# Optimization experiments

Measured on AMD Instinct MI355X. Metric: run time of the kernel, lower is better.

The kernel has to match this reference:

```python
import jax, jax.numpy as jnp
import numpy as np

B, I, H, S = 16384, 256, 256, 32
EVENT_THRESH = 0.85


def setup_inputs() -> dict:
    key = jax.random.key(0)
    ks = jax.random.split(key, 20)
    r = lambda k, shp: jax.random.normal(k, shp, dtype=jnp.float32)
    w = lambda k, shp: jax.random.normal(k, shp, dtype=jnp.float32) * 0.02
    return {
        # forward args / state
        "x_t": r(ks[0], (B, I)),
        "h_lstm": r(ks[1], (B, H)),
        "c_lstm": r(ks[2], (B, H)),
        "h_mem_prev": jnp.zeros((B, H), jnp.float32),
        "slots": r(ks[3], (B, S, I)),
        "ptr": jax.random.randint(ks[4], (B,), 0, S, dtype=jnp.int64),
        # SequenceMemoryCell params (weights stored as (in, out))
        "W_val": w(ks[5], (I, I)),
        "b_val": jnp.zeros((I,), jnp.float32),
        "W_ev": w(ks[6], (I, 1)),
        "b_ev": jnp.zeros((1,), jnp.float32),
        "pos_emb": r(ks[7], (S, I)),
        "slot_weights": jnp.ones((S,), jnp.float32),
        "W_sp": w(ks[8], (I, H)),
        "b_sp": jnp.zeros((H,), jnp.float32),
        # LSTM params
        "W_ih": w(ks[9], (I + H, 4 * H)),
        "b_ih": jnp.zeros((4 * H,), jnp.float32),
        "W_hh": w(ks[10], (H, 4 * H)),
    }


def reference(x_t, h_lstm, c_lstm, h_mem_prev, slots, ptr,
              W_val, b_val, W_ev, b_ev, pos_emb, slot_weights, W_sp, b_sp,
              W_ih, b_ih, W_hh):
    n_slots = slot_weights.shape[0]
    # --- SequenceMemoryCell ---
    e_t = jax.nn.sigmoid(x_t @ W_ev + b_ev)            # (B, 1)
    v = x_t @ W_val + b_val                            # (B, I)
    event_mask = e_t[:, 0] > EVENT_THRESH              # (B,)
    # circular-buffer scatter write at ptr, gated by event_mask
    onehot = jnp.arange(n_slots)[None, :] == ptr[:, None]          # (B, S)
    write = event_mask[:, None] & onehot                           # (B, S)
    new_slots = jnp.where(write[:, :, None], v[:, None, :], slots) # (B, S, I)
    new_ptr = (ptr + event_mask.astype(ptr.dtype)) % n_slots
    # weighted pool over slots with positional embeddings
    w = jax.nn.softmax(slot_weights)                               # (S,)
    pooled = jnp.einsum('bsi,s->bi', new_slots + pos_emb[None], w) # (B, I)
    h_mem = pooled @ W_sp + b_sp                                   # (B, H)
    # --- LSTM on [x_t; h_mem] ---
    gates = jnp.concatenate([x_t, h_mem], axis=1) @ W_ih + b_ih + h_lstm @ W_hh
    i_g, f_g, g_t, o_g = jnp.split(gates, 4, axis=1)
    c_new = jax.nn.sigmoid(f_g) * c_lstm + jax.nn.sigmoid(i_g) * jnp.tanh(g_t)
    h_new = jax.nn.sigmoid(o_g) * jnp.tanh(c_new)
    return (h_new, c_new, h_mem, new_slots, new_ptr)
```

## Files before the change

### kernel.cpp

```cpp
#include <hip/hip_runtime.h>
#include <hip/hip_bf16.h>

#define B_SZ 16384
#define I_SZ 256
#define H_SZ 256
#define S_SZ 32

typedef __attribute__((ext_vector_type(8))) short short8;
typedef __attribute__((ext_vector_type(4))) float f32x4;
typedef __attribute__((ext_vector_type(4))) short s16x4;

__device__ __forceinline__ ushort f2b(float f) {
  __hip_bfloat16 h = __float2bfloat16(f);
  return *reinterpret_cast<ushort*>(&h);
}
__device__ __forceinline__ float b2f(ushort u) {
  unsigned x = ((unsigned)u) << 16;
  float f;
  __builtin_memcpy(&f, &x, 4);
  return f;
}
__device__ __forceinline__ float sgm(float x) { return 1.0f / (1.0f + expf(-x)); }

__device__ __forceinline__ void gll16(const void* g, void* l) {
  __builtin_amdgcn_global_load_lds(
      (const __attribute__((address_space(1))) unsigned*)g,
      (__attribute__((address_space(3))) unsigned*)l, 16, 0, 0);
}

__global__ __launch_bounds__(256) void prep_weights(
    const float* __restrict__ W_sp, const float* __restrict__ W_ih,
    const float* __restrict__ W_hh, ushort* __restrict__ WspT,
    ushort* __restrict__ WcatT) {
  int idx = blockIdx.x * 256 + threadIdx.x;
  if (idx < 256 * 256) {
    int n = idx >> 8, k = idx & 255;
    WspT[idx] = f2b(W_sp[k * 256 + n]);
  } else {
    int j = idx - 256 * 256;
    int n = j / 768, k = j - n * 768;
    float v = (k < 512) ? W_ih[k * 1024 + n] : W_hh[(k - 512) * 1024 + n];
    WcatT[j] = f2b(v);
  }
}

__global__ __launch_bounds__(256) void event_pool(
    const float* __restrict__ x_t, const float* __restrict__ h_lstm,
    const float* __restrict__ slots, const int* __restrict__ ptr,
    const float* __restrict__ W_val, const float* __restrict__ b_val,
    const float* __restrict__ W_ev, const float* __restrict__ b_ev,
    const float* __restrict__ pos_emb, const float* __restrict__ slot_w,
    float* __restrict__ out_slots, float* __restrict__ out_ptr,
    ushort* __restrict__ x_b, ushort* __restrict__ hl_b,
    ushort* __restrict__ pooled_b) {
  int l = threadIdx.x & 63;
  int w = threadIdx.x >> 6;
  int b = blockIdx.x * 4 + w;
  __shared__ float x_sh[4][256];

  float4 x4 = *(const float4*)(x_t + (size_t)b * 256 + l * 4);
  *(float4*)&x_sh[w][l * 4] = x4;
  ushort4 xb = make_ushort4(f2b(x4.x), f2b(x4.y), f2b(x4.z), f2b(x4.w));
  *(ushort4*)&x_b[(size_t)b * 256 + l * 4] = xb;
  float4 hl4 = *(const float4*)(h_lstm + (size_t)b * 256 + l * 4);
  ushort4 hb = make_ushort4(f2b(hl4.x), f2b(hl4.y), f2b(hl4.z), f2b(hl4.w));
  *(ushort4*)&hl_b[(size_t)b * 256 + l * 4] = hb;

  float4 we4 = *(const float4*)(W_ev + l * 4);
  float p = x4.x * we4.x + x4.y * we4.y + x4.z * we4.z + x4.w * we4.w;
  for (int off = 32; off; off >>= 1) p += __shfl_xor(p, off, 64);
  float z = p + b_ev[0];
  bool ev = sgm(z) > 0.85f;
  int pb = ptr[b];

  __syncthreads();

  float4 v4 = make_float4(0.f, 0.f, 0.f, 0.f);
  if (ev) {
    v4 = *(const float4*)(b_val + l * 4);
    for (int k = 0; k < 256; k++) {
      float xv = x_sh[w][k];
      float4 wv = *(const float4*)(W_val + (size_t)k * 256 + l * 4);
      v4.x += xv * wv.x; v4.y += xv * wv.y;
      v4.z += xv * wv.z; v4.w += xv * wv.w;
    }
  }

  float mx = -1e30f;
  for (int s = 0; s < 32; s++) mx = fmaxf(mx, slot_w[s]);
  float sum = 0.f;
  for (int s = 0; s < 32; s++) sum += expf(slot_w[s] - mx);
  float rs = 1.f / sum;

  const float4* sl4 = (const float4*)slots + (size_t)b * 2048;
  float4* os4 = (float4*)out_slots + (size_t)b * 2048;
  const float4* pe4 = (const float4*)pos_emb;
  float4 pool = make_float4(0.f, 0.f, 0.f, 0.f);
#pragma unroll 8
  for (int s = 0; s < 32; s++) {
    float ws_ = expf(slot_w[s] - mx) * rs;
    float4 t = sl4[s * 64 + l];
    if (ev && s == pb) t = v4;
    os4[s * 64 + l] = t;
    float4 pe = pe4[s * 64 + l];
    pool.x += ws_ * (t.x + pe.x);
    pool.y += ws_ * (t.y + pe.y);
    pool.z += ws_ * (t.z + pe.z);
    pool.w += ws_ * (t.w + pe.w);
  }
  ushort4 pb4 = make_ushort4(f2b(pool.x), f2b(pool.y), f2b(pool.z), f2b(pool.w));
  *(ushort4*)&pooled_b[(size_t)b * 256 + l * 4] = pb4;

  if (l == 0) out_ptr[b] = (float)(ev ? ((pb + 1) & 31) : pb);
}

template <int KTOT, int NTOT, int EPI>
__global__ __launch_bounds__(256) void gemm_bf16(
    const ushort* __restrict__ A0, const ushort* __restrict__ A1,
    const ushort* __restrict__ A2, const ushort* __restrict__ WT,
    const float* __restrict__ bias, float* __restrict__ out_f32,
    ushort* __restrict__ out_b16) {
  int l = threadIdx.x & 63;
  int wid = threadIdx.x >> 6;
  int wm = wid >> 1, wn = wid & 1;
  int m0 = blockIdx.x * 128;
  int n0 = blockIdx.y * 128;
  __shared__ ushort Ash[128 * 32];
  __shared__ ushort Bsh[128 * 32];

  f32x4 acc[4][4] = {};

  for (int k0 = 0; k0 < KTOT; k0 += 32) {
    const ushort* As = (k0 < 256) ? A0 : ((k0 < 512) ? A1 : A2);
    int kc = k0 & 255;
#pragma unroll
    for (int i = 0; i < 2; i++) {
      int seg = i * 256 + threadIdx.x;
      int row = seg >> 2, cb = (seg & 3) * 8;
      gll16(As + (size_t)(m0 + row) * 256 + kc + cb, Ash + seg * 8);
    }
#pragma unroll
    for (int i = 0; i < 2; i++) {
      int seg = i * 256 + threadIdx.x;
      int row = seg >> 2, cb = (seg & 3) * 8;
      gll16(WT + (size_t)(n0 + row) * KTOT + k0 + cb, Bsh + seg * 8);
    }
    __syncthreads();

    short8 af[4], bfr[4];
#pragma unroll
    for (int m = 0; m < 4; m++)
      af[m] = *(const short8*)&Ash[(wm * 64 + m * 16 + (l & 15)) * 32 + (l >> 4) * 8];
#pragma unroll
    for (int n = 0; n < 4; n++)
      bfr[n] = *(const short8*)&Bsh[(wn * 64 + n * 16 + (l & 15)) * 32 + (l >> 4) * 8];
#pragma unroll
    for (int m = 0; m < 4; m++)
#pragma unroll
      for (int n = 0; n < 4; n++)
        acc[m][n] = __builtin_amdgcn_mfma_f32_16x16x32_bf16(af[m], bfr[n], acc[m][n], 0, 0, 0);
    __syncthreads();
  }

#pragma unroll
  for (int m = 0; m < 4; m++)
#pragma unroll
    for (int n = 0; n < 4; n++)
#pragma unroll
      for (int r = 0; r < 4; r++) {
        int row = m0 + wm * 64 + m * 16 + (l >> 4) * 4 + r;
        int col = n0 + wn * 64 + n * 16 + (l & 15);
        float v = acc[m][n][r] + bias[col];
        if constexpr (EPI == 0) {
          out_f32[(size_t)row * NTOT + col] = v;
          out_b16[(size_t)row * NTOT + col] = f2b(v);
        } else {
          out_b16[(size_t)row * NTOT + col] = f2b(v);
        }
      }
}

__global__ __launch_bounds__(256) void lstm_ew(
    const ushort* __restrict__ gates, const float* __restrict__ c_lstm,
    float* __restrict__ h_out, float* __restrict__ c_out) {
  int t = blockIdx.x * 256 + threadIdx.x;
  int b = t >> 6;
  int h4 = (t & 63) * 4;
  size_t g0 = (size_t)b * 1024 + h4;
  s16x4 ig = *(const s16x4*)&gates[g0];
  s16x4 fg = *(const s16x4*)&gates[g0 + 256];
  s16x4 gg = *(const s16x4*)&gates[g0 + 512];
  s16x4 og = *(const s16x4*)&gates[g0 + 768];
  float4 c = *(const float4*)&c_lstm[(size_t)b * 256 + h4];
  float4 cn, hn;
  {
    float i0 = sgm(b2f((ushort)ig[0])), f0 = sgm(b2f((ushort)fg[0]));
    float g0v = tanhf(b2f((ushort)gg[0])), o0 = sgm(b2f((ushort)og[0]));
    cn.x = f0 * c.x + i0 * g0v; hn.x = o0 * tanhf(cn.x);
  }
  {
    float i1 = sgm(b2f((ushort)ig[1])), f1 = sgm(b2f((ushort)fg[1]));
    float g1 = tanhf(b2f((ushort)gg[1])), o1 = sgm(b2f((ushort)og[1]));
    cn.y = f1 * c.y + i1 * g1; hn.y = o1 * tanhf(cn.y);
  }
  {
    float i2 = sgm(b2f((ushort)ig[2])), f2 = sgm(b2f((ushort)fg[2]));
    float g2 = tanhf(b2f((ushort)gg[2])), o2 = sgm(b2f((ushort)og[2]));
    cn.z = f2 * c.z + i2 * g2; hn.z = o2 * tanhf(cn.z);
  }
  {
    float i3 = sgm(b2f((ushort)ig[3])), f3 = sgm(b2f((ushort)fg[3]));
    float g3 = tanhf(b2f((ushort)gg[3])), o3 = sgm(b2f((ushort)og[3]));
    cn.w = f3 * c.w + i3 * g3; hn.w = o3 * tanhf(cn.w);
  }
  size_t o = (size_t)b * 256 + h4;
  *(float4*)&c_out[o] = cn;
  *(float4*)&h_out[o] = hn;
}

extern "C" void kernel_launch(void* const* d_in, const int* in_sizes, int n_in,
                              void* d_out, int out_size, void* d_ws, size_t ws_size,
                              hipStream_t stream) {
  const float* x_t    = (const float*)d_in[0];
  const float* h_lstm = (const float*)d_in[1];
  const float* c_lstm = (const float*)d_in[2];
  const float* slots  = (const float*)d_in[4];
  const int*   ptr    = (const int*)d_in[5];
  const float* W_val  = (const float*)d_in[6];
  const float* b_val  = (const float*)d_in[7];
  const float* W_ev   = (const float*)d_in[8];
  const float* b_ev   = (const float*)d_in[9];
  const float* pos_emb = (const float*)d_in[10];
  const float* slot_w  = (const float*)d_in[11];
  const float* W_sp   = (const float*)d_in[12];
  const float* b_sp   = (const float*)d_in[13];
  const float* W_ih   = (const float*)d_in[14];
  const float* b_ih   = (const float*)d_in[15];
  const float* W_hh   = (const float*)d_in[16];

  float* out = (float*)d_out;
  const size_t BH = (size_t)B_SZ * H_SZ;
  float* out_h    = out;
  float* out_c    = out + BH;
  float* out_hmem = out + 2 * BH;
  float* out_slots = out + 3 * BH;
  float* out_ptr   = out + 3 * BH + (size_t)B_SZ * S_SZ * I_SZ;

  char* ws = (char*)d_ws;
  ushort* x_b      = (ushort*)(ws);
  ushort* hl_b     = (ushort*)(ws + 8388608);
  ushort* pooled_b = (ushort*)(ws + 16777216);
  ushort* hmem_b   = (ushort*)(ws + 25165824);
  ushort* WspT     = (ushort*)(ws + 33554432);
  ushort* WcatT    = (ushort*)(ws + 33685504);
  ushort* gates    = (ushort*)(ws + 35258368);

  prep_weights<<<3328, 256, 0, stream>>>(W_sp, W_ih, W_hh, WspT, WcatT);

  event_pool<<<B_SZ / 4, 256, 0, stream>>>(
      x_t, h_lstm, slots, ptr, W_val, b_val, W_ev, b_ev, pos_emb, slot_w,
      out_slots, out_ptr, x_b, hl_b, pooled_b);

  gemm_bf16<256, 256, 0><<<dim3(128, 2), 256, 0, stream>>>(
      pooled_b, pooled_b, pooled_b, WspT, b_sp, out_hmem, hmem_b);

  gemm_bf16<768, 1024, 1><<<dim3(128, 8), 256, 0, stream>>>(
      x_b, hmem_b, hl_b, WcatT, b_ih, nullptr, gates);

  lstm_ew<<<B_SZ * 64 / 256, 256, 0, stream>>>(gates, c_lstm, out_h, out_c);
}
```

Before: 309.0 us.

## Fuse LSTM elementwise into gate GEMM epilogue via interleaved weight columns

Reorders the columns of the concatenated LSTM weight so each wave's 64-column slice holds the i, f, g and o gates for the same 16 hidden units. The LSTM cell update can then run directly in the GEMM epilogue, which removes the bf16 gates buffer round-trip and the separate lstm_ew launch. Gates now stay in fp32 rather than being rounded to bf16. The epilogue now reads c_lstm and writes h and c with 16-lane strided scalar accesses, which are less coalesced than the old float4 accesses.

Result: no change. 304.9 us (-1.3%).

```diff
diff --git a/kernel.cpp b/kernel.cpp
--- a/kernel.cpp
+++ b/kernel.cpp
@@ -8,17 +8,10 @@
 
 typedef __attribute__((ext_vector_type(8))) short short8;
 typedef __attribute__((ext_vector_type(4))) float f32x4;
-typedef __attribute__((ext_vector_type(4))) short s16x4;
 
 __device__ __forceinline__ ushort f2b(float f) {
   __hip_bfloat16 h = __float2bfloat16(f);
   return *reinterpret_cast<ushort*>(&h);
-}
-__device__ __forceinline__ float b2f(ushort u) {
-  unsigned x = ((unsigned)u) << 16;
-  float f;
-  __builtin_memcpy(&f, &x, 4);
-  return f;
 }
 __device__ __forceinline__ float sgm(float x) { return 1.0f / (1.0f + expf(-x)); }
 
@@ -38,7 +31,9 @@
     WspT[idx] = f2b(W_sp[k * 256 + n]);
   } else {
     int j = idx - 256 * 256;
-    int n = j / 768, k = j - n * 768;
+    int r = j / 768, k = j - r * 768;
+    int hb = r >> 6, g = (r >> 4) & 3, hl = r & 15;
+    int n = g * 256 + hb * 16 + hl;
     float v = (k < 512) ? W_ih[k * 1024 + n] : W_hh[(k - 512) * 1024 + n];
     WcatT[j] = f2b(v);
   }
@@ -119,7 +114,8 @@
     const ushort* __restrict__ A0, const ushort* __restrict__ A1,
     const ushort* __restrict__ A2, const ushort* __restrict__ WT,
     const float* __restrict__ bias, float* __restrict__ out_f32,
-    ushort* __restrict__ out_b16) {
+    ushort* __restrict__ out_b16, const float* __restrict__ c_lstm,
+    float* __restrict__ h_out, float* __restrict__ c_out) {
   int l = threadIdx.x & 63;
   int wid = threadIdx.x >> 6;
   int wm = wid >> 1, wn = wid & 1;
@@ -162,60 +158,38 @@
     __syncthreads();
   }
 
-#pragma unroll
-  for (int m = 0; m < 4; m++)
-#pragma unroll
-    for (int n = 0; n < 4; n++)
+  if constexpr (EPI == 0) {
+#pragma unroll
+    for (int m = 0; m < 4; m++)
+#pragma unroll
+      for (int n = 0; n < 4; n++)
+#pragma unroll
+        for (int r = 0; r < 4; r++) {
+          int row = m0 + wm * 64 + m * 16 + (l >> 4) * 4 + r;
+          int col = n0 + wn * 64 + n * 16 + (l & 15);
+          float v = acc[m][n][r] + bias[col];
+          out_f32[(size_t)row * NTOT + col] = v;
+          out_b16[(size_t)row * NTOT + col] = f2b(v);
+        }
+  } else {
+    int h = ((n0 >> 6) + wn) * 16 + (l & 15);
+    float bi = bias[h], bf_ = bias[256 + h], bg = bias[512 + h], bo = bias[768 + h];
+#pragma unroll
+    for (int m = 0; m < 4; m++)
 #pragma unroll
       for (int r = 0; r < 4; r++) {
         int row = m0 + wm * 64 + m * 16 + (l >> 4) * 4 + r;
-        int col = n0 + wn * 64 + n * 16 + (l & 15);
-        float v = acc[m][n][r] + bias[col];
-        if constexpr (EPI == 0) {
-          out_f32[(size_t)row * NTOT + col] = v;
-          out_b16[(size_t)row * NTOT + col] = f2b(v);
-        } else {
-          out_b16[(size_t)row * NTOT + col] = f2b(v);
-        }
+        float ig = acc[m][0][r] + bi;
+        float fg = acc[m][1][r] + bf_;
+        float gt = acc[m][2][r] + bg;
+        float og = acc[m][3][r] + bo;
+        float c = c_lstm[(size_t)row * 256 + h];
+        float cn = sgm(fg) * c + sgm(ig) * tanhf(gt);
+        float hn = sgm(og) * tanhf(cn);
+        c_out[(size_t)row * 256 + h] = cn;
+        h_out[(size_t)row * 256 + h] = hn;
       }
-}
-
-__global__ __launch_bounds__(256) void lstm_ew(
-    const ushort* __restrict__ gates, const float* __restrict__ c_lstm,
-    float* __restrict__ h_out, float* __restrict__ c_out) {
-  int t = blockIdx.x * 256 + threadIdx.x;
-  int b = t >> 6;
-  int h4 = (t & 63) * 4;
-  size_t g0 = (size_t)b * 1024 + h4;
-  s16x4 ig = *(const s16x4*)&gates[g0];
-  s16x4 fg = *(const s16x4*)&gates[g0 + 256];
-  s16x4 gg = *(const s16x4*)&gates[g0 + 512];
-  s16x4 og = *(const s16x4*)&gates[g0 + 768];
-  float4 c = *(const float4*)&c_lstm[(size_t)b * 256 + h4];
-  float4 cn, hn;
-  {
-    float i0 = sgm(b2f((ushort)ig[0])), f0 = sgm(b2f((ushort)fg[0]));
-    float g0v = tanhf(b2f((ushort)gg[0])), o0 = sgm(b2f((ushort)og[0]));
-    cn.x = f0 * c.x + i0 * g0v; hn.x = o0 * tanhf(cn.x);
-  }
-  {
-    float i1 = sgm(b2f((ushort)ig[1])), f1 = sgm(b2f((ushort)fg[1]));
-    float g1 = tanhf(b2f((ushort)gg[1])), o1 = sgm(b2f((ushort)og[1]));
-    cn.y = f1 * c.y + i1 * g1; hn.y = o1 * tanhf(cn.y);
-  }
-  {
-    float i2 = sgm(b2f((ushort)ig[2])), f2 = sgm(b2f((ushort)fg[2]));
-    float g2 = tanhf(b2f((ushort)gg[2])), o2 = sgm(b2f((ushort)og[2]));
-    cn.z = f2 * c.z + i2 * g2; hn.z = o2 * tanhf(cn.z);
-  }
-  {
-    float i3 = sgm(b2f((ushort)ig[3])), f3 = sgm(b2f((ushort)fg[3]));
-    float g3 = tanhf(b2f((ushort)gg[3])), o3 = sgm(b2f((ushort)og[3]));
-    cn.w = f3 * c.w + i3 * g3; hn.w = o3 * tanhf(cn.w);
-  }
-  size_t o = (size_t)b * 256 + h4;
-  *(float4*)&c_out[o] = cn;
-  *(float4*)&h_out[o] = hn;
+  }
 }
 
 extern "C" void kernel_launch(void* const* d_in, const int* in_sizes, int n_in,
@@ -253,7 +227,6 @@
   ushort* hmem_b   = (ushort*)(ws + 25165824);
   ushort* WspT     = (ushort*)(ws + 33554432);
   ushort* WcatT    = (ushort*)(ws + 33685504);
-  ushort* gates    = (ushort*)(ws + 35258368);
 
   prep_weights<<<3328, 256, 0, stream>>>(W_sp, W_ih, W_hh, WspT, WcatT);
 
@@ -262,10 +235,10 @@
       out_slots, out_ptr, x_b, hl_b, pooled_b);
 
   gemm_bf16<256, 256, 0><<<dim3(128, 2), 256, 0, stream>>>(
-      pooled_b, pooled_b, pooled_b, WspT, b_sp, out_hmem, hmem_b);
-
-  gemm_bf16<768, 1024, 1><<<dim3(128, 8), 256, 0, stream>>>(
-      x_b, hmem_b, hl_b, WcatT, b_ih, nullptr, gates);
-
-  lstm_ew<<<B_SZ * 64 / 256, 256, 0, stream>>>(gates, c_lstm, out_h, out_c);
-}
+      pooled_b, pooled_b, pooled_b, WspT, b_sp, out_hmem, hmem_b,
+      nullptr, nullptr, nullptr);
+
+  gemm_bf16<768, 1024, 2><<<dim3(128, 8), 256, 0, stream>>>(
+      x_b, hmem_b, hl_b, WcatT, b_ih, nullptr, nullptr,
+      c_lstm, out_h, out_c);
+}
```
